# Kernel tuning notes

Hardware: AMD Instinct MI355X
Metric: run time of the kernel (lower is better)

## Reference

```python
import jax, jax.numpy as jnp
import numpy as np

N, FIN, FOUT = 4096, 512, 256
ALPHA = 0.2          # LeakyReLU negative slope
NEG_INF = -9e15      # mask value from the torch source


def setup_inputs() -> dict:
    key = jax.random.key(0)
    ks = jax.random.split(key, 11)
    h = jax.random.normal(ks[0], (N, FIN), dtype=jnp.float32)
    adj_n = jax.random.randint(ks[1], (N, N), 0, 2, dtype=jnp.int32)
    adj_d = jax.random.randint(ks[2], (N, N), 0, 2, dtype=jnp.int32)
    G_nd = jax.random.normal(ks[3], (2, N, FOUT), dtype=jnp.float32)
    # learned parameters (xavier-ish scale)
    W_n = jax.random.normal(ks[4], (FIN, FOUT), dtype=jnp.float32) * 0.05
    a1_n = jax.random.normal(ks[5], (FOUT, 1), dtype=jnp.float32) * 0.05
    a2_n = jax.random.normal(ks[6], (FOUT, 1), dtype=jnp.float32) * 0.05
    W_d = jax.random.normal(ks[7], (FIN, FOUT), dtype=jnp.float32) * 0.05
    a1_d = jax.random.normal(ks[8], (FOUT, 1), dtype=jnp.float32) * 0.05
    a2_d = jax.random.normal(ks[9], (FOUT, 1), dtype=jnp.float32) * 0.05
    scale = jnp.zeros((1,), dtype=jnp.float32)
    return {"h": h, "adj_n": adj_n, "adj_d": adj_d, "G_nd": G_nd,
            "W_n": W_n, "a1_n": a1_n, "a2_n": a2_n,
            "W_d": W_d, "a1_d": a1_d, "a2_d": a2_d, "scale": scale}


def _gat(h, adj, W, a1, a2):
    # Wh: [N, FOUT]
    Wh = h @ W
    # outer-sum attention logits: e[i,j] = leakyrelu(Wh_i.a1 + Wh_j.a2)
    e = jax.nn.leaky_relu((Wh @ a1) + (Wh @ a2).T, negative_slope=ALPHA)  # [N, N]
    att = jnp.where(adj > 0, e, jnp.float32(NEG_INF))
    att = jax.nn.softmax(att, axis=-1)
    # dropout is identity in eval mode
    return jax.nn.elu(att @ Wh)  # [N, FOUT]


def reference(h, adj_n, adj_d, G_nd, W_n, a1_n, a2_n, W_d, a1_d, a2_d, scale):
    f_n_S = _gat(h, adj_n, W_n, a1_n, a2_n)
    f_d_S = _gat(h, adj_d, W_d, a1_d, a2_d)
    # The G_nd cross-attention branch (f_nd_C) in the torch source is computed
    # but never used in the returned value; omitted here (jit would DCE it).
    return f_n_S + f_d_S
```

## Files before the change

kernel.cpp:

```cpp
#include <hip/hip_runtime.h>

#define N_NODES 4096
#define FIN     512
#define FOUT    256
#define NSPLIT  4
#define NTILES  ((N_NODES / NSPLIT) / 64)

typedef __attribute__((ext_vector_type(8))) short bf16x8s;
typedef __attribute__((ext_vector_type(4))) float f32x4;
typedef __attribute__((ext_vector_type(8))) unsigned short u16x8;
typedef unsigned short u16;
typedef unsigned int   u32;
typedef unsigned long long u64;

__device__ inline u16 f2b(float f) {
    union { float f; unsigned int u; } v; v.f = f;
    unsigned int r = v.u + 0x7fffu + ((v.u >> 16) & 1u);
    return (u16)(r >> 16);
}

__global__ __launch_bounds__(256) void prep_kernel(
    const float* __restrict__ h, const float* __restrict__ Wn,
    const float* __restrict__ Wd,
    const int* __restrict__ adjn, const int* __restrict__ adjd,
    u16* __restrict__ hb, u16* __restrict__ WTb, u64* __restrict__ bits64,
    float* __restrict__ s12)
{
    __shared__ u16 tl[64 * 72];
    const int t = threadIdx.x;
    const int bid = blockIdx.x;

    if (bid < 1024) {
        int idx = (bid * 256 + t) * 8;
        float4 f0 = *(const float4*)&h[idx];
        float4 f1 = *(const float4*)&h[idx + 4];
        u16x8 o;
        o[0]=f2b(f0.x); o[1]=f2b(f0.y); o[2]=f2b(f0.z); o[3]=f2b(f0.w);
        o[4]=f2b(f1.x); o[5]=f2b(f1.y); o[6]=f2b(f1.z); o[7]=f2b(f1.w);
        *(u16x8*)&hb[idx] = o;
    } else if (bid < 2048) {
        const int lane = t & 63;
        const long base0 = ((long)(bid - 1024) * 4 + (t >> 6)) * 8192;
        #pragma unroll 2
        for (int it = 0; it < 32; ++it) {
            long base = base0 + (long)it * 256;
            const int* p = (base < (1L << 24)) ? (adjn + base)
                                               : (adjd + (base - (1L << 24)));
            int v0 = p[lane], v1 = p[lane + 64], v2 = p[lane + 128], v3 = p[lane + 192];
            u64 b0 = __ballot(v0 > 0);
            u64 b1 = __ballot(v1 > 0);
            u64 b2 = __ballot(v2 > 0);
            u64 b3 = __ballot(v3 > 0);
            if (lane == 0) {
                u64* d = bits64 + (base >> 6);
                d[0] = b0; d[1] = b1; d[2] = b2; d[3] = b3;
            }
        }
    } else if (bid < 2112) {
        int id = bid - 2048;
        int kx = id & 7, ny = (id >> 3) & 3, b = id >> 5;
        const float* W = b ? Wd : Wn;
        int k0 = kx * 64, n0 = ny * 64;
        int kr = t >> 2, nc0 = (t & 3) * 16;
        const float* src = W + (size_t)(k0 + kr) * FOUT + n0 + nc0;
        #pragma unroll
        for (int jv = 0; jv < 4; ++jv) {
            float4 f = *(const float4*)(src + jv * 4);
            tl[(nc0 + jv * 4 + 0) * 72 + kr] = f2b(f.x);
            tl[(nc0 + jv * 4 + 1) * 72 + kr] = f2b(f.y);
            tl[(nc0 + jv * 4 + 2) * 72 + kr] = f2b(f.z);
            tl[(nc0 + jv * 4 + 3) * 72 + kr] = f2b(f.w);
        }
        __syncthreads();
        int n = t >> 2, kc0 = (t & 3) * 16;
        u16* dst = WTb + ((size_t)b << 17) + (size_t)(n0 + n) * FIN + k0 + kc0;
        *(uint4*)dst       = *(uint4*)&tl[n * 72 + kc0];
        *(uint4*)(dst + 8) = *(uint4*)&tl[n * 72 + kc0 + 8];
    } else {
        float4 z = {0.f, 0.f, 0.f, 0.f};
        float4* p4 = (float4*)s12;
        #pragma unroll
        for (int k = 0; k < 16; ++k) p4[k * 256 + t] = z;
    }
}

__global__ __launch_bounds__(256) void wh_gemm_kernel(
    const u16* __restrict__ hb, const u16* __restrict__ WTb,
    const float* __restrict__ a1n, const float* __restrict__ a2n,
    const float* __restrict__ a1d, const float* __restrict__ a2d,
    u16* __restrict__ WhT, float* __restrict__ s1, float* __restrict__ s2)
{
    __shared__ u16 smem[8192];
    u16* a_lds = smem;
    u16* b_lds = smem + 4096;

    const int t = threadIdx.x, lane = t & 63, w = t >> 6;
    const int q = lane >> 4, ln = lane & 15;
    const int i0 = blockIdx.x * 64, n0 = blockIdx.y * 64, b = blockIdx.z;
    const u16* wt = WTb + ((size_t)b << 17);

    f32x4 acc[4];
    #pragma unroll
    for (int i = 0; i < 4; ++i) acc[i] = (f32x4){0.f, 0.f, 0.f, 0.f};

    for (int kt = 0; kt < 8; ++kt) {
        const int k0 = kt * 64;
        __syncthreads();
        #pragma unroll
        for (int it = 0; it < 2; ++it) {
            int chunk = it * 256 + t;
            int r = chunk >> 3, kc = chunk & 7;
            const u16* g = hb + (size_t)(i0 + r) * FIN + k0 + ((kc ^ (r & 7)) * 8);
            u16* l = a_lds + (it * 256 + w * 64) * 8;
            __builtin_amdgcn_global_load_lds(
                (const __attribute__((address_space(1))) void*)g,
                (__attribute__((address_space(3))) void*)l, 16, 0, 0);
        }
        #pragma unroll
        for (int it = 0; it < 2; ++it) {
            int chunk = it * 256 + t;
            int n = chunk >> 3, kc = chunk & 7;
            const u16* g = wt + (size_t)(n0 + n) * FIN + k0 + ((kc ^ (n & 7)) * 8);
            u16* l = b_lds + (it * 256 + w * 64) * 8;
            __builtin_amdgcn_global_load_lds(
                (const __attribute__((address_space(1))) void*)g,
                (__attribute__((address_space(3))) void*)l, 16, 0, 0);
        }
        __syncthreads();
        #pragma unroll
        for (int ks = 0; ks < 2; ++ks) {
            int sw = ((ks * 4 + q) ^ (ln & 7)) * 8;
            bf16x8s af = *(const bf16x8s*)&a_lds[(w * 16 + ln) * 64 + sw];
            #pragma unroll
            for (int nt = 0; nt < 4; ++nt) {
                bf16x8s bfv = *(const bf16x8s*)&b_lds[(nt * 16 + ln) * 64 + sw];
                acc[nt] = __builtin_amdgcn_mfma_f32_16x16x32_bf16(af, bfv, acc[nt], 0, 0, 0);
            }
        }
    }

    {
        const float* a1 = b ? a1d : a1n;
        const float* a2 = b ? a2d : a2n;
        float s1p[4] = {0.f, 0.f, 0.f, 0.f};
        float s2p[4] = {0.f, 0.f, 0.f, 0.f};
        #pragma unroll
        for (int nt = 0; nt < 4; ++nt) {
            float va1 = a1[n0 + nt * 16 + ln];
            float va2 = a2[n0 + nt * 16 + ln];
            #pragma unroll
            for (int r = 0; r < 4; ++r) {
                s1p[r] += acc[nt][r] * va1;
                s2p[r] += acc[nt][r] * va2;
            }
        }
        #pragma unroll
        for (int r = 0; r < 4; ++r) {
            #pragma unroll
            for (int off = 8; off >= 1; off >>= 1) {
                s1p[r] += __shfl_xor(s1p[r], off);
                s2p[r] += __shfl_xor(s2p[r], off);
            }
            if (ln == 0) {
                int row = i0 + w * 16 + q * 4 + r;
                atomicAdd(&s1[b * N_NODES + row], s1p[r]);
                atomicAdd(&s2[b * N_NODES + row], s2p[r]);
            }
        }
    }

    __syncthreads();
    #pragma unroll
    for (int nt = 0; nt < 4; ++nt)
        #pragma unroll
        for (int r = 0; r < 4; ++r)
            smem[(nt * 16 + ln) * 72 + (w * 16 + q * 4 + r)] = f2b(acc[nt][r]);
    __syncthreads();
    {
        const int nl = t >> 2, is = (t & 3) * 16;
        u16* dst = WhT + ((size_t)b << 20) + (size_t)(n0 + nl) * N_NODES + i0 + is;
        *(uint4*)dst       = *(uint4*)&smem[nl * 72 + is];
        *(uint4*)(dst + 8) = *(uint4*)&smem[nl * 72 + is + 8];
    }
}

__global__ __launch_bounds__(256, 4) void attn_kernel(
    const u32* __restrict__ bits,
    const u16* __restrict__ WhT,
    const float* __restrict__ s1, const float* __restrict__ s2,
    float* __restrict__ num_ws, float* __restrict__ den_ws)
{
    __shared__ u16 wht_lds[256 * 64];
    __shared__ u16 p_lds[32 * 64];
    __shared__ float den_lds[32];

    const int t = threadIdx.x, lane = t & 63, w = t >> 6;
    const int q = lane >> 4, ln = lane & 15;
    const int b = blockIdx.z, split = blockIdx.y;
    const int i0 = blockIdx.x * 32;

    const u16* whtB = WhT + ((size_t)b << 20);
    const float* s1b = s1 + b * N_NODES;
    const float* s2b = s2 + b * N_NODES;

    const int pr = t >> 3;
    const int cw = t & 7;
    const int pc = cw * 8;
    const int bsh = (cw & 3) * 8;
    const float s1v = s1b[i0 + pr];
    const u32* bitrow = bits + (size_t)b * (N_NODES * N_NODES / 32)
                             + (size_t)(i0 + pr) * (N_NODES / 32) + (cw >> 2);

    if (t < 32) den_lds[t] = 0.f;

    f32x4 acc[2][4];
    #pragma unroll
    for (int mt = 0; mt < 2; ++mt)
        #pragma unroll
        for (int nt = 0; nt < 4; ++nt) acc[mt][nt] = (f32x4){0.f, 0.f, 0.f, 0.f};

    const int jbase = split * (N_NODES / NSPLIT);
    u32 bw_pf = bitrow[jbase >> 5];
    float4 sv0_pf = *(const float4*)&s2b[jbase + pc];
    float4 sv1_pf = *(const float4*)&s2b[jbase + pc + 4];

    for (int jt = 0; jt < NTILES; ++jt) {
        const int j0 = jbase + jt * 64;
        __syncthreads();
        #pragma unroll
        for (int it = 0; it < 8; ++it) {
            int chunk = it * 256 + t;
            int n = chunk >> 3, kc = chunk & 7;
            const u16* g = whtB + (size_t)n * N_NODES + j0 + ((kc ^ (n & 7)) * 8);
            u16* l = wht_lds + (it * 256 + w * 64) * 8;
            __builtin_amdgcn_global_load_lds(
                (const __attribute__((address_space(1))) void*)g,
                (__attribute__((address_space(3))) void*)l, 16, 0, 0);
        }
        u32 bw = bw_pf;
        float4 sv0 = sv0_pf, sv1 = sv1_pf;
        if (jt < NTILES - 1) {
            bw_pf = bitrow[(j0 + 64) >> 5];
            sv0_pf = *(const float4*)&s2b[j0 + 64 + pc];
            sv1_pf = *(const float4*)&s2b[j0 + 64 + pc + 4];
        }
        u32 mask8 = (bw >> bsh) & 0xffu;
        float svf[8] = {sv0.x, sv0.y, sv0.z, sv0.w, sv1.x, sv1.y, sv1.z, sv1.w};
        float den_part = 0.f;
        u16x8 pk;
        #pragma unroll
        for (int jj = 0; jj < 8; ++jj) {
            float x = s1v + svf[jj];
            float lr = fmaxf(x, 0.2f * x);
            float p = ((mask8 >> jj) & 1u) ? __expf(lr) : 0.f;
            den_part += p;
            pk[jj] = f2b(p);
        }
        den_part += __shfl_down(den_part, 4, 8);
        den_part += __shfl_down(den_part, 2, 8);
        den_part += __shfl_down(den_part, 1, 8);
        if ((t & 7) == 0) den_lds[pr] += den_part;
        *(u16x8*)&p_lds[pr * 64 + ((cw ^ (pr & 7)) * 8)] = pk;
        __syncthreads();
        #pragma unroll
        for (int ks = 0; ks < 2; ++ks) {
            int sw = ((ks * 4 + q) ^ (ln & 7)) * 8;
            bf16x8s a0  = *(const bf16x8s*)&p_lds[ln * 64 + sw];
            bf16x8s a1f = *(const bf16x8s*)&p_lds[(16 + ln) * 64 + sw];
            #pragma unroll
            for (int nt = 0; nt < 4; ++nt) {
                bf16x8s bfv = *(const bf16x8s*)&wht_lds[(w * 64 + nt * 16 + ln) * 64 + sw];
                acc[0][nt] = __builtin_amdgcn_mfma_f32_16x16x32_bf16(a0,  bfv, acc[0][nt], 0, 0, 0);
                acc[1][nt] = __builtin_amdgcn_mfma_f32_16x16x32_bf16(a1f, bfv, acc[1][nt], 0, 0, 0);
            }
        }
    }
    const size_t pbase = (size_t)(b * NSPLIT + split) * N_NODES;
    #pragma unroll
    for (int mt = 0; mt < 2; ++mt)
        #pragma unroll
        for (int r = 0; r < 4; ++r) {
            int row = mt * 16 + q * 4 + r;
            #pragma unroll
            for (int nt = 0; nt < 4; ++nt)
                num_ws[(pbase + i0 + row) * FOUT + w * 64 + nt * 16 + ln] = acc[mt][nt][r];
        }
    if (t < 32) den_ws[pbase + i0 + t] = den_lds[t];
}

__global__ __launch_bounds__(256) void reduce_kernel(
    const float* __restrict__ num_ws, const float* __restrict__ den_ws,
    float* __restrict__ out)
{
    int gid = blockIdx.x * 256 + threadIdx.x;
    int i = gid >> 6;
    int f4 = (gid & 63) * 4;
    float4 o = {0.f, 0.f, 0.f, 0.f};
    #pragma unroll
    for (int b = 0; b < 2; ++b) {
        float4 num = {0.f, 0.f, 0.f, 0.f};
        float den = 0.f;
        #pragma unroll
        for (int s = 0; s < NSPLIT; ++s) {
            const float4 v = *(const float4*)&num_ws[((size_t)(b * NSPLIT + s) * N_NODES + i) * FOUT + f4];
            num.x += v.x; num.y += v.y; num.z += v.z; num.w += v.w;
            den += den_ws[(size_t)(b * NSPLIT + s) * N_NODES + i];
        }
        float inv = 1.0f / den;
        float e0 = num.x * inv, e1 = num.y * inv, e2 = num.z * inv, e3 = num.w * inv;
        o.x += (e0 > 0.f) ? e0 : expm1f(e0);
        o.y += (e1 > 0.f) ? e1 : expm1f(e1);
        o.z += (e2 > 0.f) ? e2 : expm1f(e2);
        o.w += (e3 > 0.f) ? e3 : expm1f(e3);
    }
    *(float4*)&out[(size_t)i * FOUT + f4] = o;
}

extern "C" void kernel_launch(void* const* d_in, const int* in_sizes, int n_in,
                              void* d_out, int out_size, void* d_ws, size_t ws_size,
                              hipStream_t stream) {
    const float* h    = (const float*)d_in[0];
    const int*   adjn = (const int*)d_in[1];
    const int*   adjd = (const int*)d_in[2];
    const float* Wn   = (const float*)d_in[4];
    const float* a1n  = (const float*)d_in[5];
    const float* a2n  = (const float*)d_in[6];
    const float* Wd   = (const float*)d_in[7];
    const float* a1d  = (const float*)d_in[8];
    const float* a2d  = (const float*)d_in[9];

    char* ws = (char*)d_ws;
    u16*  WhT  = (u16*)ws;
    u32*  bits = (u32*)(ws + ((size_t)4 << 20));
    float* s1  = (float*)(ws + ((size_t)8 << 20));
    float* s2  = s1 + 2 * N_NODES;
    float* den = s2 + 2 * N_NODES;
    u16*  hb   = (u16*)(ws + ((size_t)8 << 20) + ((size_t)256 << 10));
    u16*  WTb  = (u16*)(ws + ((size_t)12 << 20) + ((size_t)256 << 10));
    float* num = (float*)(ws + ((size_t)8 << 20) + ((size_t)256 << 10));

    prep_kernel<<<2113, 256, 0, stream>>>(h, Wn, Wd, adjn, adjd, hb, WTb, (u64*)bits, s1);
    wh_gemm_kernel<<<dim3(64, 4, 2), 256, 0, stream>>>(hb, WTb, a1n, a2n, a1d, a2d, WhT, s1, s2);
    attn_kernel<<<dim3(128, NSPLIT, 2), 256, 0, stream>>>(bits, WhT, s1, s2, num, den);
    reduce_kernel<<<1024, 256, 0, stream>>>(num, den, (float*)d_out);
}
```

Before: 228.3 us.

## Double attention row tile and repack adjacency bits with vector loads

The attention kernel now handles 64 query rows per block instead of 32. Each WhT tile staged in LDS therefore feeds twice as many MFMAs, and the number of blocks re-reading WhT is halved. The adjacency bit-packing step now has each lane load 16 consecutive ints as int4 and write a 16-bit mask, replacing the wave-ballot scheme, and uses twice as many blocks. In exchange, the attention grid halves to 512 blocks and accumulator registers double, so occupancy and latency hiding may suffer.

```diff
diff --git a/kernel.cpp b/kernel.cpp
--- a/kernel.cpp
+++ b/kernel.cpp
@@ -23,7 +23,7 @@
     const float* __restrict__ h, const float* __restrict__ Wn,
     const float* __restrict__ Wd,
     const int* __restrict__ adjn, const int* __restrict__ adjd,
-    u16* __restrict__ hb, u16* __restrict__ WTb, u64* __restrict__ bits64,
+    u16* __restrict__ hb, u16* __restrict__ WTb, u16* __restrict__ bits16,
     float* __restrict__ s12)
 {
     __shared__ u16 tl[64 * 72];
@@ -38,26 +38,33 @@
         o[0]=f2b(f0.x); o[1]=f2b(f0.y); o[2]=f2b(f0.z); o[3]=f2b(f0.w);
         o[4]=f2b(f1.x); o[5]=f2b(f1.y); o[6]=f2b(f1.z); o[7]=f2b(f1.w);
         *(u16x8*)&hb[idx] = o;
-    } else if (bid < 2048) {
-        const int lane = t & 63;
-        const long base0 = ((long)(bid - 1024) * 4 + (t >> 6)) * 8192;
-        #pragma unroll 2
-        for (int it = 0; it < 32; ++it) {
-            long base = base0 + (long)it * 256;
-            const int* p = (base < (1L << 24)) ? (adjn + base)
-                                               : (adjd + (base - (1L << 24)));
-            int v0 = p[lane], v1 = p[lane + 64], v2 = p[lane + 128], v3 = p[lane + 192];
-            u64 b0 = __ballot(v0 > 0);
-            u64 b1 = __ballot(v1 > 0);
-            u64 b2 = __ballot(v2 > 0);
-            u64 b3 = __ballot(v3 > 0);
-            if (lane == 0) {
-                u64* d = bits64 + (base >> 6);
-                d[0] = b0; d[1] = b1; d[2] = b2; d[3] = b3;
-            }
-        }
-    } else if (bid < 2112) {
-        int id = bid - 2048;
+    } else if (bid < 3072) {
+        const int lane = t & 63, w = t >> 6;
+        const long gw = (long)(bid - 1024) * 4 + w;
+        const long base = gw * 4096;
+        const int* p = (base < (1L << 24)) ? (adjn + base)
+                                           : (adjd + (base - (1L << 24)));
+        const int4* src = (const int4*)p + lane * 4;
+        u16* dst = bits16 + (base >> 4) + lane;
+        #pragma unroll
+        for (int s = 0; s < 4; ++s) {
+            int4 a = src[s * 256 + 0];
+            int4 b = src[s * 256 + 1];
+            int4 c = src[s * 256 + 2];
+            int4 d = src[s * 256 + 3];
+            u32 m = 0;
+            m |= (u32)(a.x > 0) << 0;  m |= (u32)(a.y > 0) << 1;
+            m |= (u32)(a.z > 0) << 2;  m |= (u32)(a.w > 0) << 3;
+            m |= (u32)(b.x > 0) << 4;  m |= (u32)(b.y > 0) << 5;
+            m |= (u32)(b.z > 0) << 6;  m |= (u32)(b.w > 0) << 7;
+            m |= (u32)(c.x > 0) << 8;  m |= (u32)(c.y > 0) << 9;
+            m |= (u32)(c.z > 0) << 10; m |= (u32)(c.w > 0) << 11;
+            m |= (u32)(d.x > 0) << 12; m |= (u32)(d.y > 0) << 13;
+            m |= (u32)(d.z > 0) << 14; m |= (u32)(d.w > 0) << 15;
+            dst[s * 64] = (u16)m;
+        }
+    } else if (bid < 3136) {
+        int id = bid - 3072;
         int kx = id & 7, ny = (id >> 3) & 3, b = id >> 5;
         const float* W = b ? Wd : Wn;
         int k0 = kx * 64, n0 = ny * 64;
@@ -184,20 +191,20 @@
     }
 }
 
-__global__ __launch_bounds__(256, 4) void attn_kernel(
+__global__ __launch_bounds__(256) void attn_kernel(
     const u32* __restrict__ bits,
     const u16* __restrict__ WhT,
     const float* __restrict__ s1, const float* __restrict__ s2,
     float* __restrict__ num_ws, float* __restrict__ den_ws)
 {
     __shared__ u16 wht_lds[256 * 64];
-    __shared__ u16 p_lds[32 * 64];
-    __shared__ float den_lds[32];
+    __shared__ u16 p_lds[64 * 64];
+    __shared__ float den_lds[64];
 
     const int t = threadIdx.x, lane = t & 63, w = t >> 6;
     const int q = lane >> 4, ln = lane & 15;
     const int b = blockIdx.z, split = blockIdx.y;
-    const int i0 = blockIdx.x * 32;
+    const int i0 = blockIdx.x * 64;
 
     const u16* whtB = WhT + ((size_t)b << 20);
     const float* s1b = s1 + b * N_NODES;
@@ -207,20 +214,23 @@
     const int cw = t & 7;
     const int pc = cw * 8;
     const int bsh = (cw & 3) * 8;
-    const float s1v = s1b[i0 + pr];
-    const u32* bitrow = bits + (size_t)b * (N_NODES * N_NODES / 32)
-                             + (size_t)(i0 + pr) * (N_NODES / 32) + (cw >> 2);
-
-    if (t < 32) den_lds[t] = 0.f;
-
-    f32x4 acc[2][4];
-    #pragma unroll
-    for (int mt = 0; mt < 2; ++mt)
+    const float s1v0 = s1b[i0 + pr];
+    const float s1v1 = s1b[i0 + pr + 32];
+    const u32* bitrow0 = bits + (size_t)b * (N_NODES * (N_NODES / 32))
+                              + (size_t)(i0 + pr) * (N_NODES / 32) + (cw >> 2);
+    const u32* bitrow1 = bitrow0 + 32 * (N_NODES / 32);
+
+    if (t < 64) den_lds[t] = 0.f;
+
+    f32x4 acc[4][4];
+    #pragma unroll
+    for (int mt = 0; mt < 4; ++mt)
         #pragma unroll
         for (int nt = 0; nt < 4; ++nt) acc[mt][nt] = (f32x4){0.f, 0.f, 0.f, 0.f};
 
     const int jbase = split * (N_NODES / NSPLIT);
-    u32 bw_pf = bitrow[jbase >> 5];
+    u32 bw0_pf = bitrow0[jbase >> 5];
+    u32 bw1_pf = bitrow1[jbase >> 5];
     float4 sv0_pf = *(const float4*)&s2b[jbase + pc];
     float4 sv1_pf = *(const float4*)&s2b[jbase + pc + 4];
 
@@ -237,47 +247,55 @@
                 (const __attribute__((address_space(1))) void*)g,
                 (__attribute__((address_space(3))) void*)l, 16, 0, 0);
         }
-        u32 bw = bw_pf;
+        u32 bw0 = bw0_pf, bw1 = bw1_pf;
         float4 sv0 = sv0_pf, sv1 = sv1_pf;
         if (jt < NTILES - 1) {
-            bw_pf = bitrow[(j0 + 64) >> 5];
+            bw0_pf = bitrow0[(j0 + 64) >> 5];
+            bw1_pf = bitrow1[(j0 + 64) >> 5];
             sv0_pf = *(const float4*)&s2b[j0 + 64 + pc];
             sv1_pf = *(const float4*)&s2b[j0 + 64 + pc + 4];
         }
-        u32 mask8 = (bw >> bsh) & 0xffu;
+        u32 m0 = (bw0 >> bsh) & 0xffu;
+        u32 m1 = (bw1 >> bsh) & 0xffu;
         float svf[8] = {sv0.x, sv0.y, sv0.z, sv0.w, sv1.x, sv1.y, sv1.z, sv1.w};
-        float den_part = 0.f;
-        u16x8 pk;
+        float d0 = 0.f, d1 = 0.f;
+        u16x8 pk0, pk1;
         #pragma unroll
         for (int jj = 0; jj < 8; ++jj) {
-            float x = s1v + svf[jj];
-            float lr = fmaxf(x, 0.2f * x);
-            float p = ((mask8 >> jj) & 1u) ? __expf(lr) : 0.f;
-            den_part += p;
-            pk[jj] = f2b(p);
-        }
-        den_part += __shfl_down(den_part, 4, 8);
-        den_part += __shfl_down(den_part, 2, 8);
-        den_part += __shfl_down(den_part, 1, 8);
-        if ((t & 7) == 0) den_lds[pr] += den_part;
-        *(u16x8*)&p_lds[pr * 64 + ((cw ^ (pr & 7)) * 8)] = pk;
+            float sv = svf[jj];
+            float x0 = s1v0 + sv, x1 = s1v1 + sv;
+            float p0 = ((m0 >> jj) & 1u) ? __expf(fmaxf(x0, 0.2f * x0)) : 0.f;
+            float p1 = ((m1 >> jj) & 1u) ? __expf(fmaxf(x1, 0.2f * x1)) : 0.f;
+            d0 += p0; d1 += p1;
+            pk0[jj] = f2b(p0); pk1[jj] = f2b(p1);
+        }
+        d0 += __shfl_down(d0, 4, 8); d1 += __shfl_down(d1, 4, 8);
+        d0 += __shfl_down(d0, 2, 8); d1 += __shfl_down(d1, 2, 8);
+        d0 += __shfl_down(d0, 1, 8); d1 += __shfl_down(d1, 1, 8);
+        if ((t & 7) == 0) { den_lds[pr] += d0; den_lds[pr + 32] += d1; }
+        int swp = ((cw ^ (pr & 7)) * 8);
+        *(u16x8*)&p_lds[pr * 64 + swp] = pk0;
+        *(u16x8*)&p_lds[(pr + 32) * 64 + swp] = pk1;
         __syncthreads();
         #pragma unroll
         for (int ks = 0; ks < 2; ++ks) {
             int sw = ((ks * 4 + q) ^ (ln & 7)) * 8;
-            bf16x8s a0  = *(const bf16x8s*)&p_lds[ln * 64 + sw];
-            bf16x8s a1f = *(const bf16x8s*)&p_lds[(16 + ln) * 64 + sw];
+            bf16x8s af[4];
+            #pragma unroll
+            for (int mt = 0; mt < 4; ++mt)
+                af[mt] = *(const bf16x8s*)&p_lds[(mt * 16 + ln) * 64 + sw];
             #pragma unroll
             for (int nt = 0; nt < 4; ++nt) {
                 bf16x8s bfv = *(const bf16x8s*)&wht_lds[(w * 64 + nt * 16 + ln) * 64 + sw];
-                acc[0][nt] = __builtin_amdgcn_mfma_f32_16x16x32_bf16(a0,  bfv, acc[0][nt], 0, 0, 0);
-                acc[1][nt] = __builtin_amdgcn_mfma_f32_16x16x32_bf16(a1f, bfv, acc[1][nt], 0, 0, 0);
+                #pragma unroll
+                for (int mt = 0; mt < 4; ++mt)
+                    acc[mt][nt] = __builtin_amdgcn_mfma_f32_16x16x32_bf16(af[mt], bfv, acc[mt][nt], 0, 0, 0);
             }
         }
     }
     const size_t pbase = (size_t)(b * NSPLIT + split) * N_NODES;
     #pragma unroll
-    for (int mt = 0; mt < 2; ++mt)
+    for (int mt = 0; mt < 4; ++mt)
         #pragma unroll
         for (int r = 0; r < 4; ++r) {
             int row = mt * 16 + q * 4 + r;
@@ -285,7 +303,7 @@
             for (int nt = 0; nt < 4; ++nt)
                 num_ws[(pbase + i0 + row) * FOUT + w * 64 + nt * 16 + ln] = acc[mt][nt][r];
         }
-    if (t < 32) den_ws[pbase + i0 + t] = den_lds[t];
+    if (t < 64) den_ws[pbase + i0 + t] = den_lds[t];
 }
 
 __global__ __launch_bounds__(256) void reduce_kernel(
@@ -331,7 +349,7 @@
 
     char* ws = (char*)d_ws;
     u16*  WhT  = (u16*)ws;
-    u32*  bits = (u32*)(ws + ((size_t)4 << 20));
+    u16*  bits = (u16*)(ws + ((size_t)4 << 20));
     float* s1  = (float*)(ws + ((size_t)8 << 20));
     float* s2  = s1 + 2 * N_NODES;
     float* den = s2 + 2 * N_NODES;
@@ -339,8 +357,8 @@
     u16*  WTb  = (u16*)(ws + ((size_t)12 << 20) + ((size_t)256 << 10));
     float* num = (float*)(ws + ((size_t)8 << 20) + ((size_t)256 << 10));
 
-    prep_kernel<<<2113, 256, 0, stream>>>(h, Wn, Wd, adjn, adjd, hb, WTb, (u64*)bits, s1);
+    prep_kernel<<<3137, 256, 0, stream>>>(h, Wn, Wd, adjn, adjd, hb, WTb, bits, s1);
     wh_gemm_kernel<<<dim3(64, 4, 2), 256, 0, stream>>>(hb, WTb, a1n, a2n, a1d, a2d, WhT, s1, s2);
-    attn_kernel<<<dim3(128, NSPLIT, 2), 256, 0, stream>>>(bits, WhT, s1, s2, num, den);
+    attn_kernel<<<dim3(64, NSPLIT, 2), 256, 0, stream>>>((const u32*)bits, WhT, s1, s2, num, den);
     reduce_kernel<<<1024, 256, 0, stream>>>(num, den, (float*)d_out);
 }
```

Result: faster. 221.5 us (-3.0%).
